# Performance work log

Measured on AMD Instinct MI355X. Metric: run time of the kernel, lower is better.

## Reference

```python
import jax, jax.numpy as jnp
import numpy as np

N, S, H, D = 2, 1024, 12, 64
HIDDEN = H * D
EPS = 1e-6


def setup_inputs() -> dict:
    key = jax.random.key(0)
    k1, k2, k3 = jax.random.split(key, 3)
    return {
        "q": jax.random.normal(k1, (N, S, H, D), dtype=jnp.float32),
        "v": jax.random.normal(k2, (N, S, H, D), dtype=jnp.float32),
        "attention_mask": jnp.ones((N, S), dtype=jnp.float32),
        "head_mask": jnp.ones((H,), dtype=jnp.float32),
        "pos_weight": jax.random.normal(k3, (S, HIDDEN), dtype=jnp.float32),
    }


def reference(q, v, attention_mask, head_mask, pos_weight):
    seq_len = q.shape[1]
    # transpose_for_scores: [S, hidden] -> [S, H, D]
    p = pos_weight[:seq_len].reshape(seq_len, H, D)
    # elu feature map: elu(x) + 1
    p = jax.nn.elu(p) + 1.0
    # broadcast to batch and apply padding mask: [N, S, H, D]
    p = p[None, :, :, :] * attention_mask[:, :, None, None]
    # pv: [N, H, M, D]
    pv = jnp.einsum('nshd,nshm->nhmd', p, v)
    pv = pv * head_mask[None, :, None, None]
    # ppv: [N, L, H, M, D]
    ppv = jnp.einsum('nlhd,nhmd->nlhmd', p, pv)
    # normalizer z_pp: [N, L, H]
    z_pp = jnp.einsum('nlhd,nhd->nlh', p, p.sum(axis=1)) + EPS
    return ppv, z_pp
```

## Files before the change

### kernel.cpp

```cpp
#include <hip/hip_runtime.h>
#include <math.h>

#define N_  2
#define S_  1024
#define H_  12
#define D_  64
#define HIDDEN_ 768
#define EPS_ 1e-6f

#define CHUNK 64
#define NS    (S_/CHUNK)

#define LT 16
#define NL (S_/LT)

__device__ __forceinline__ float elup1(float x) {
    return x > 0.0f ? x + 1.0f : __expf(x);
}

__global__ __launch_bounds__(256) void pv_kernel(
        const float* __restrict__ v,
        const float* __restrict__ mask,
        const float* __restrict__ w,
        float* __restrict__ pv_part,
        float* __restrict__ psum_part) {
    __shared__ float p_lds[CHUNK * 64];
    __shared__ float v_lds[CHUNK * 64];

    const int b  = blockIdx.x;
    const int sc = b % NS;
    const int h  = (b / NS) % H_;
    const int n  = b / (NS * H_);
    const int s0 = sc * CHUNK;
    const int t  = threadIdx.x;

    for (int j = t; j < CHUNK * 16; j += 256) {
        const int row = j >> 4;
        const int c4  = (j & 15) * 4;
        const int s   = s0 + row;
        const float m = mask[n * S_ + s];
        const float4 wv = *(const float4*)(w + (size_t)s * HIDDEN_ + h * 64 + c4);
        float4 p;
        p.x = elup1(wv.x) * m;
        p.y = elup1(wv.y) * m;
        p.z = elup1(wv.z) * m;
        p.w = elup1(wv.w) * m;
        *(float4*)(p_lds + row * 64 + c4) = p;
        const float4 vv = *(const float4*)(v + (((size_t)n * S_ + s) * H_ + h) * 64 + c4);
        *(float4*)(v_lds + row * 64 + c4) = vv;
    }
    __syncthreads();

    const int d  = t & 63;
    const int mq = t >> 6;
    float acc[16];
    #pragma unroll
    for (int i = 0; i < 16; ++i) acc[i] = 0.0f;
    float ps = 0.0f;

    for (int s = 0; s < CHUNK; ++s) {
        const float pd = p_lds[s * 64 + d];
        ps += pd;
        const float* vr = v_lds + s * 64 + mq * 16;
        #pragma unroll
        for (int i = 0; i < 16; ++i)
            acc[i] = fmaf(pd, vr[i], acc[i]);
    }

    float* pvp = pv_part + (((size_t)(n * H_ + h)) * NS + sc) * (64 * 64);
    #pragma unroll
    for (int i = 0; i < 16; ++i)
        pvp[(mq * 16 + i) * 64 + d] = acc[i];
    if (mq == 0)
        psum_part[(((size_t)(n * H_ + h)) * NS + sc) * 64 + d] = ps;
}

__global__ __launch_bounds__(256) void reduce_z_kernel(
        const float* __restrict__ pv_part,
        const float* __restrict__ psum_part,
        const float* __restrict__ w,
        const float* __restrict__ mask,
        float* __restrict__ pv_ws,
        float* __restrict__ z_out) {
    __shared__ float psum_lds[64];

    const int b  = blockIdx.x;
    const int q  = b & 3;
    const int h  = (b >> 2) % H_;
    const int n  = b / (4 * H_);
    const int nh = n * H_ + h;
    const int t  = threadIdx.x;

    if (t < 64) {
        const float* ps = psum_part + (size_t)nh * NS * 64 + t;
        float s = 0.0f;
        #pragma unroll
        for (int sc = 0; sc < NS; ++sc)
            s += ps[sc * 64];
        psum_lds[t] = s;
    }

    const float* src = pv_part + (size_t)nh * NS * 4096 + q * 1024;
    float* dst = pv_ws + (size_t)nh * 4096 + q * 1024;
    #pragma unroll
    for (int k = 0; k < 4; ++k) {
        const int e = t + k * 256;
        float s = 0.0f;
        #pragma unroll
        for (int sc = 0; sc < NS; ++sc)
            s += src[(size_t)sc * 4096 + e];
        dst[e] = s;
    }
    __syncthreads();

    const int l = q * 256 + t;
    const float m = mask[n * S_ + l];
    const float4* wr = (const float4*)(w + (size_t)l * HIDDEN_ + h * 64);
    float acc = 0.0f;
    #pragma unroll
    for (int i = 0; i < 16; ++i) {
        const float4 wv = wr[i];
        acc += elup1(wv.x) * psum_lds[i * 4 + 0];
        acc += elup1(wv.y) * psum_lds[i * 4 + 1];
        acc += elup1(wv.z) * psum_lds[i * 4 + 2];
        acc += elup1(wv.w) * psum_lds[i * 4 + 3];
    }
    z_out[(n * S_ + l) * H_ + h] = acc * m + EPS_;
}

__global__ __launch_bounds__(256) void ppv_kernel(
        const float* __restrict__ w,
        const float* __restrict__ mask,
        const float* __restrict__ head_mask,
        const float* __restrict__ pv_ws,
        float* __restrict__ ppv_out) {
    __shared__ float p_lds[LT * 64];

    const int b  = blockIdx.x;
    const int h  = b % H_;
    const int lb = (b / H_) % NL;
    const int n  = b / (H_ * NL);
    const int l0 = lb * LT;
    const int t  = threadIdx.x;

    const float hm = head_mask[h];
    const float4* pv4 = (const float4*)(pv_ws + ((size_t)(n * H_ + h)) * 4096);
    float4 pr[4];
    #pragma unroll
    for (int jj = 0; jj < 4; ++jj) {
        float4 vv = pv4[t + jj * 256];
        vv.x *= hm; vv.y *= hm; vv.z *= hm; vv.w *= hm;
        pr[jj] = vv;
    }

    const int d  = t & 63;
    const int lw = t >> 6;
    #pragma unroll
    for (int lq = 0; lq < LT / 4; ++lq) {
        const int l = lq * 4 + lw;
        const float m = mask[n * S_ + l0 + l];
        p_lds[l * 64 + d] =
            elup1(w[(size_t)(l0 + l) * HIDDEN_ + h * 64 + d]) * m;
    }
    __syncthreads();

    const int d0 = (t * 4) & 63;
    float4* outb = (float4*)ppv_out + ((size_t)(n * S_ + l0) * H_ + h) * 1024;
    #pragma unroll 4
    for (int l = 0; l < LT; ++l) {
        const float4 pw = *(const float4*)(p_lds + l * 64 + d0);
        float4* o = outb + (size_t)l * (H_ * 1024);
        #pragma unroll
        for (int jj = 0; jj < 4; ++jj) {
            float4 r;
            r.x = pw.x * pr[jj].x;
            r.y = pw.y * pr[jj].y;
            r.z = pw.z * pr[jj].z;
            r.w = pw.w * pr[jj].w;
            o[t + jj * 256] = r;
        }
    }
}

extern "C" void kernel_launch(void* const* d_in, const int* in_sizes, int n_in,
                              void* d_out, int out_size, void* d_ws, size_t ws_size,
                              hipStream_t stream) {
    const float* v     = (const float*)d_in[1];
    const float* mask  = (const float*)d_in[2];
    const float* hmask = (const float*)d_in[3];
    const float* w     = (const float*)d_in[4];
    float* out = (float*)d_out;

    float* pv_part   = (float*)d_ws;
    float* psum_part = pv_part + (size_t)N_ * H_ * NS * 64 * 64;
    float* pv_ws     = psum_part + (size_t)N_ * H_ * NS * 64;

    float* z_out = out + (size_t)N_ * S_ * H_ * 64 * 64;

    pv_kernel<<<dim3(N_ * H_ * NS), dim3(256), 0, stream>>>(
        v, mask, w, pv_part, psum_part);

    reduce_z_kernel<<<dim3(N_ * H_ * 4), dim3(256), 0, stream>>>(
        pv_part, psum_part, w, mask, pv_ws, z_out);

    ppv_kernel<<<dim3(N_ * H_ * NL), dim3(256), 0, stream>>>(
        w, mask, hmask, pv_ws, out);
}
```

Measured before the change: 432.2 us.

## Fuse partial reduction and z normalizer into ppv kernel, double row tile

Removes the separate reduce kernel: each ppv block now sums the 16 pv partial chunks and psum partials itself, scales by head_mask, and computes z for its rows from the p tile already in LDS. LT doubles to 32 so the redundant per-block reduction (16×16KB reads per block) is amortized over more output rows, and a block-index swizzle groups blocks sharing the same (n,h) across XCDs for L2 reuse. This saves one launch and the pv_ws round trip, at the cost of redundant partial-sum reads (768 blocks each reading 256KB, mostly L2-served) and a serial 64-length dot product for z in a few threads.

```diff
diff --git a/kernel.cpp b/kernel.cpp
--- a/kernel.cpp
+++ b/kernel.cpp
@@ -11,7 +11,7 @@
 #define CHUNK 64
 #define NS    (S_/CHUNK)
 
-#define LT 16
+#define LT 32
 #define NL (S_/LT)
 
 __device__ __forceinline__ float elup1(float x) {
@@ -75,82 +75,49 @@
         psum_part[(((size_t)(n * H_ + h)) * NS + sc) * 64 + d] = ps;
 }
 
-__global__ __launch_bounds__(256) void reduce_z_kernel(
+__global__ __launch_bounds__(256) void ppv_fused_kernel(
         const float* __restrict__ pv_part,
         const float* __restrict__ psum_part,
         const float* __restrict__ w,
         const float* __restrict__ mask,
-        float* __restrict__ pv_ws,
+        const float* __restrict__ head_mask,
+        float* __restrict__ ppv_out,
         float* __restrict__ z_out) {
+    __shared__ float p_lds[LT * 64];
     __shared__ float psum_lds[64];
 
-    const int b  = blockIdx.x;
-    const int q  = b & 3;
-    const int h  = (b >> 2) % H_;
-    const int n  = b / (4 * H_);
-    const int nh = n * H_ + h;
+    const int bid = blockIdx.x;
+    const int wk  = (bid & 7) * 96 + (bid >> 3);
+
+    const int lb = wk % NL;
+    const int g  = wk / NL;
+    const int h  = g % H_;
+    const int n  = g / H_;
+    const int l0 = lb * LT;
     const int t  = threadIdx.x;
 
+    const float hm = head_mask[h];
+    const float4* part4 = (const float4*)(pv_part + (size_t)g * NS * 4096);
+    float4 pr[4];
+    #pragma unroll
+    for (int jj = 0; jj < 4; ++jj) {
+        float4 s = make_float4(0.f, 0.f, 0.f, 0.f);
+        #pragma unroll
+        for (int sc = 0; sc < NS; ++sc) {
+            const float4 v4 = part4[sc * 1024 + t + jj * 256];
+            s.x += v4.x; s.y += v4.y; s.z += v4.z; s.w += v4.w;
+        }
+        s.x *= hm; s.y *= hm; s.z *= hm; s.w *= hm;
+        pr[jj] = s;
+    }
+
     if (t < 64) {
-        const float* ps = psum_part + (size_t)nh * NS * 64 + t;
+        const float* ps = psum_part + (size_t)g * NS * 64 + t;
         float s = 0.0f;
         #pragma unroll
         for (int sc = 0; sc < NS; ++sc)
             s += ps[sc * 64];
         psum_lds[t] = s;
-    }
-
-    const float* src = pv_part + (size_t)nh * NS * 4096 + q * 1024;
-    float* dst = pv_ws + (size_t)nh * 4096 + q * 1024;
-    #pragma unroll
-    for (int k = 0; k < 4; ++k) {
-        const int e = t + k * 256;
-        float s = 0.0f;
-        #pragma unroll
-        for (int sc = 0; sc < NS; ++sc)
-            s += src[(size_t)sc * 4096 + e];
-        dst[e] = s;
-    }
-    __syncthreads();
-
-    const int l = q * 256 + t;
-    const float m = mask[n * S_ + l];
-    const float4* wr = (const float4*)(w + (size_t)l * HIDDEN_ + h * 64);
-    float acc = 0.0f;
-    #pragma unroll
-    for (int i = 0; i < 16; ++i) {
-        const float4 wv = wr[i];
-        acc += elup1(wv.x) * psum_lds[i * 4 + 0];
-        acc += elup1(wv.y) * psum_lds[i * 4 + 1];
-        acc += elup1(wv.z) * psum_lds[i * 4 + 2];
-        acc += elup1(wv.w) * psum_lds[i * 4 + 3];
-    }
-    z_out[(n * S_ + l) * H_ + h] = acc * m + EPS_;
-}
-
-__global__ __launch_bounds__(256) void ppv_kernel(
-        const float* __restrict__ w,
-        const float* __restrict__ mask,
-        const float* __restrict__ head_mask,
-        const float* __restrict__ pv_ws,
-        float* __restrict__ ppv_out) {
-    __shared__ float p_lds[LT * 64];
-
-    const int b  = blockIdx.x;
-    const int h  = b % H_;
-    const int lb = (b / H_) % NL;
-    const int n  = b / (H_ * NL);
-    const int l0 = lb * LT;
-    const int t  = threadIdx.x;
-
-    const float hm = head_mask[h];
-    const float4* pv4 = (const float4*)(pv_ws + ((size_t)(n * H_ + h)) * 4096);
-    float4 pr[4];
-    #pragma unroll
-    for (int jj = 0; jj < 4; ++jj) {
-        float4 vv = pv4[t + jj * 256];
-        vv.x *= hm; vv.y *= hm; vv.z *= hm; vv.w *= hm;
-        pr[jj] = vv;
     }
 
     const int d  = t & 63;
@@ -163,6 +130,14 @@
             elup1(w[(size_t)(l0 + l) * HIDDEN_ + h * 64 + d]) * m;
     }
     __syncthreads();
+
+    if (t < LT) {
+        float z = 0.0f;
+        #pragma unroll
+        for (int dd = 0; dd < 64; ++dd)
+            z += p_lds[t * 64 + dd] * psum_lds[dd];
+        z_out[((size_t)n * S_ + l0 + t) * H_ + h] = z + EPS_;
+    }
 
     const int d0 = (t * 4) & 63;
     float4* outb = (float4*)ppv_out + ((size_t)(n * S_ + l0) * H_ + h) * 1024;
@@ -193,16 +168,12 @@
 
     float* pv_part   = (float*)d_ws;
     float* psum_part = pv_part + (size_t)N_ * H_ * NS * 64 * 64;
-    float* pv_ws     = psum_part + (size_t)N_ * H_ * NS * 64;
 
     float* z_out = out + (size_t)N_ * S_ * H_ * 64 * 64;
 
     pv_kernel<<<dim3(N_ * H_ * NS), dim3(256), 0, stream>>>(
         v, mask, w, pv_part, psum_part);
 
-    reduce_z_kernel<<<dim3(N_ * H_ * 4), dim3(256), 0, stream>>>(
-        pv_part, psum_part, w, mask, pv_ws, z_out);
-
-    ppv_kernel<<<dim3(N_ * H_ * NL), dim3(256), 0, stream>>>(
-        w, mask, hmask, pv_ws, out);
+    ppv_fused_kernel<<<dim3(N_ * H_ * NL), dim3(256), 0, stream>>>(
+        pv_part, psum_part, w, mask, hmask, out, z_out);
 }
```

Result: slower. 442.5 us (+2.4%).
